# Kernel optimization log

Measured on AMD Instinct MI355X. Metric: run time of the kernel, lower is better.

The kernel has to match this reference:

```python
import jax, jax.numpy as jnp
import numpy as np

B, S, Db, E, T = 64, 512, 768, 50, 68
NC, NT, K, V = 16, 8, 3, 100
MAXLEN = 8


def _make_spans(k1, k2, n):
    starts = jax.random.randint(k1, (B, n), 0, S - MAXLEN)
    lens = jax.random.randint(k2, (B, n), 1, MAXLEN + 1)
    return jnp.stack([starts, starts + lens], axis=-1)  # [B,n,2] half-open


def setup_inputs() -> dict:
    key = jax.random.key(0)
    ks = jax.random.split(key, 12)
    enc = jax.random.normal(ks[0], (B, S, Db), jnp.float32)
    entity_table = jax.random.normal(ks[1], (V, E), jnp.float32) * 0.02
    entity_table = entity_table.at[0].set(0.0)  # padding_idx=0
    fc1_w = jax.random.normal(ks[2], (Db, Db + E), jnp.float32) * 0.02
    fc1_b = jnp.zeros((Db,), jnp.float32)
    trig_w = jax.random.normal(ks[3], (T, Db), jnp.float32) * 0.02
    trig_b = jnp.zeros((T,), jnp.float32)
    entities_x = jax.random.randint(ks[4], (B, S, K), 0, V)
    head_idx = jax.random.randint(ks[5], (B, S), 0, S)
    cand_spans = _make_spans(ks[6], ks[7], NC)
    trig_spans = _make_spans(ks[8], ks[9], NT)
    return {"enc": enc, "entity_table": entity_table, "fc1_w": fc1_w,
            "fc1_b": fc1_b, "trig_w": trig_w, "trig_b": trig_b,
            "entities_x": entities_x, "head_idx": head_idx,
            "cand_spans": cand_spans, "trig_spans": trig_spans}


def _span_mean(x, spans):
    # x: [B,S,D], spans: [B,N,2] half-open -> [B,N,D] mean over span tokens
    pos = jnp.arange(x.shape[1])
    mask = (pos[None, None, :] >= spans[..., 0:1]) & (pos[None, None, :] < spans[..., 1:2])
    m = mask.astype(x.dtype)  # [B,N,S]
    cnt = jnp.maximum(m.sum(-1, keepdims=True), 1.0)
    return jnp.einsum('bns,bsd->bnd', m, x) / cnt


def reference(enc, entity_table, fc1_w, fc1_b, trig_w, trig_b,
              entities_x, head_idx, cand_spans, trig_spans):
    # multi-label entity embedding: sum over K label slots (padding row is zero)
    ent = entity_table[entities_x].sum(axis=2)            # [B,S,E]
    x = jnp.concatenate([enc, ent], axis=-1)              # [B,S,Db+E]
    x = jax.nn.relu(jnp.einsum('bsd,hd->bsh', x, fc1_w) + fc1_b)  # fc1 (dropout=eval)
    # per-sample index_select over sequence dim (wordpiece head gather)
    x = jnp.take_along_axis(x, head_idx[:, :, None], axis=1)      # [B,S,768]
    trigger_logits = jnp.einsum('bsh,th->bst', x, trig_w) + trig_b  # [B,S,T]
    trigger_hat = jnp.argmax(trigger_logits, axis=-1)
    # span mean-pooling for predicted triggers and golden entity candidates
    ev = _span_mean(x, trig_spans)                        # [B,NT,768]
    en = _span_mean(x, cand_spans)                        # [B,NC,768]
    ev_e = jnp.broadcast_to(ev[:, :, None, :], (B, NT, NC, Db))
    en_e = jnp.broadcast_to(en[:, None, :, :], (B, NT, NC, Db))
    argument_hidden = jnp.concatenate([ev_e, en_e], axis=-1)  # [B,NT,NC,1536]
    return trigger_logits, trigger_hat, argument_hidden
```

## Files before the change

kernel.cpp:

```cpp
#include <hip/hip_runtime.h>

#define BS_TOTAL 32768
#define DB 768
#define KV 832
#define KREAL 818
#define TT 68
#define SEQ 512

typedef float v2f __attribute__((ext_vector_type(2)));
typedef float f32x4 __attribute__((ext_vector_type(4)));
typedef _Float16 f16x8 __attribute__((ext_vector_type(8)));
typedef _Float16 f16x4 __attribute__((ext_vector_type(4)));
typedef unsigned int uint;
typedef unsigned short ushort;

union U4 { uint4 u; f16x8 h; };

__device__ __forceinline__ _Float16 us2h(ushort x){ union{ushort u;_Float16 h;}c; c.u=x; return c.h; }
__device__ __forceinline__ ushort h2us(_Float16 x){ union{ushort u;_Float16 h;}c; c.h=x; return c.u; }
__device__ __forceinline__ uint packx(float xs){
    _Float16 h=(_Float16)xs; _Float16 l=(_Float16)(xs-(float)h);
    return (uint)h2us(h) | ((uint)h2us(l)<<16);
}

__global__ __launch_bounds__(256) void splitw_kernel(
    const float* __restrict__ W, const float* __restrict__ Wt,
    _Float16* __restrict__ W0, _Float16* __restrict__ W1,
    _Float16* __restrict__ T0, _Float16* __restrict__ T1)
{
    int row = blockIdx.x;
    int t = threadIdx.x;
    if (row < DB) {
        int c4 = t * 4;
        if (c4 < KV) {
#pragma unroll
            for (int j = 0; j < 4; ++j) {
                int k = c4 + j;
                float v = (k < KREAL) ? W[(size_t)row * KREAL + k] * 1024.f : 0.f;
                _Float16 h = (_Float16)v;
                W0[(size_t)row * KV + k] = h;
                W1[(size_t)row * KV + k] = (_Float16)(v - (float)h);
            }
        }
    } else {
        int r2 = row - DB;
#pragma unroll
        for (int j = 0; j < 3; ++j) {
            int k = t * 3 + j;
            if (k < DB) {
                float v = (r2 < TT) ? Wt[(size_t)r2 * DB + k] * 1024.f : 0.f;
                _Float16 h = (_Float16)v;
                T0[(size_t)r2 * DB + k] = h;
                T1[(size_t)r2 * DB + k] = (_Float16)(v - (float)h);
            }
        }
    }
}

__global__ __launch_bounds__(256, 2) void fc1_mfma(
    const float* __restrict__ enc, const int* __restrict__ ex,
    const float* __restrict__ table,
    const _Float16* __restrict__ W0, const _Float16* __restrict__ W1,
    const float* __restrict__ bias, uint* __restrict__ xout)
{
    __shared__ char lds[65536];
    char* sA0 = lds;
    char* sA1 = lds + 16384;
    char* sW0 = lds + 32768;
    char* sW1 = lds + 49152;
    const int t = threadIdx.x;
    const int l = t & 63;
    const int w = t >> 6;
    const int wr = w >> 1, wc = w & 1;
    const int bm0 = blockIdx.x * 128;
    const int bn0 = blockIdx.y * 128;

    f32x4 acc[4][4];
#pragma unroll
    for (int i = 0; i < 4; ++i)
#pragma unroll
        for (int j = 0; j < 4; ++j) acc[i][j] = (f32x4){0.f, 0.f, 0.f, 0.f};

    float4 pa[8];
    uint4 pw0[4], pw1[4];

    auto loadA = [&](int k0) {
        if (k0 < DB) {
#pragma unroll
            for (int c = 0; c < 8; ++c) {
                int idx = t + c * 256;
                int r = idx >> 4;
                int c4 = (idx & 15) << 2;
                pa[c] = *reinterpret_cast<const float4*>(enc + (size_t)(bm0 + r) * DB + k0 + c4);
            }
        } else {
#pragma unroll
            for (int c = 0; c < 8; ++c) {
                int idx = t + c * 256;
                int r = idx >> 4;
                int c4 = (idx & 15) << 2;
                const int* exr = ex + (size_t)(bm0 + r) * 3;
                int i0 = exr[0] * 50, i1 = exr[1] * 50, i2 = exr[2] * 50;
                float vv[4];
#pragma unroll
                for (int j = 0; j < 4; ++j) {
                    int e = c4 + j;
                    vv[j] = (e < 50) ? (table[i0 + e] + table[i1 + e] + table[i2 + e]) : 0.f;
                }
                pa[c] = make_float4(vv[0], vv[1], vv[2], vv[3]);
            }
        }
    };
    auto loadW = [&](int k0) {
#pragma unroll
        for (int c = 0; c < 4; ++c) {
            int idx = t + c * 256;
            int r = idx >> 3;
            int h0 = (idx & 7) << 3;
            pw0[c] = *reinterpret_cast<const uint4*>(W0 + (size_t)(bn0 + r) * KV + k0 + h0);
            pw1[c] = *reinterpret_cast<const uint4*>(W1 + (size_t)(bn0 + r) * KV + k0 + h0);
        }
    };

    loadA(0); loadW(0);

    for (int kt = 0; kt < 13; ++kt) {
        __syncthreads();
#pragma unroll
        for (int c = 0; c < 8; ++c) {
            int idx = t + c * 256;
            int r = idx >> 4;
            int b0 = (idx & 15) << 3;
            int off = (r << 7) + (b0 ^ ((r & 7) << 4));
            float f0 = pa[c].x * 32.f, f1 = pa[c].y * 32.f;
            float f2 = pa[c].z * 32.f, f3 = pa[c].w * 32.f;
            _Float16 h0 = (_Float16)f0, h1 = (_Float16)f1, h2 = (_Float16)f2, h3 = (_Float16)f3;
            f16x4 hi = {h0, h1, h2, h3};
            f16x4 lo = {(_Float16)(f0 - (float)h0), (_Float16)(f1 - (float)h1),
                        (_Float16)(f2 - (float)h2), (_Float16)(f3 - (float)h3)};
            *reinterpret_cast<f16x4*>(sA0 + off) = hi;
            *reinterpret_cast<f16x4*>(sA1 + off) = lo;
        }
#pragma unroll
        for (int c = 0; c < 4; ++c) {
            int idx = t + c * 256;
            int r = idx >> 3;
            int b0 = (idx & 7) << 4;
            int off = (r << 7) + (b0 ^ ((r & 7) << 4));
            *reinterpret_cast<uint4*>(sW0 + off) = pw0[c];
            *reinterpret_cast<uint4*>(sW1 + off) = pw1[c];
        }
        __syncthreads();
        if (kt < 12) { loadA((kt + 1) * 64); loadW((kt + 1) * 64); }
#pragma unroll
        for (int ks = 0; ks < 2; ++ks) {
            const int lr = l & 15;
            const int kb = ks * 64 + ((l >> 4) << 4);
            f16x8 a0f[4], a1f[4], b0f[4], b1f[4];
#pragma unroll
            for (int mf = 0; mf < 4; ++mf) {
                int r = wr * 64 + mf * 16 + lr;
                int off = (r << 7) + (kb ^ ((r & 7) << 4));
                a0f[mf] = *reinterpret_cast<const f16x8*>(sA0 + off);
                a1f[mf] = *reinterpret_cast<const f16x8*>(sA1 + off);
            }
#pragma unroll
            for (int nf = 0; nf < 4; ++nf) {
                int r = wc * 64 + nf * 16 + lr;
                int off = (r << 7) + (kb ^ ((r & 7) << 4));
                b0f[nf] = *reinterpret_cast<const f16x8*>(sW0 + off);
                b1f[nf] = *reinterpret_cast<const f16x8*>(sW1 + off);
            }
#pragma unroll
            for (int mf = 0; mf < 4; ++mf)
#pragma unroll
                for (int nf = 0; nf < 4; ++nf) {
                    acc[mf][nf] = __builtin_amdgcn_mfma_f32_16x16x32_f16(a0f[mf], b0f[nf], acc[mf][nf], 0, 0, 0);
                    acc[mf][nf] = __builtin_amdgcn_mfma_f32_16x16x32_f16(a1f[mf], b0f[nf], acc[mf][nf], 0, 0, 0);
                    acc[mf][nf] = __builtin_amdgcn_mfma_f32_16x16x32_f16(a0f[mf], b1f[nf], acc[mf][nf], 0, 0, 0);
                }
        }
    }

    const float inv = 1.0f / 32768.f;
#pragma unroll
    for (int nf = 0; nf < 4; ++nf) {
        int col = bn0 + wc * 64 + nf * 16 + (l & 15);
        float bv = bias[col];
#pragma unroll
        for (int mf = 0; mf < 4; ++mf) {
            int rbase = bm0 + wr * 64 + mf * 16 + ((l >> 4) << 2);
#pragma unroll
            for (int j = 0; j < 4; ++j) {
                float x = fmaxf(acc[mf][nf][j] * inv + bv, 0.f);
                xout[(size_t)(rbase + j) * DB + col] = packx(x * 256.f);
            }
        }
    }
}

__global__ __launch_bounds__(256, 4) void trig_mfma(
    const uint* __restrict__ xfc, const int* __restrict__ head_idx,
    const _Float16* __restrict__ T0, const _Float16* __restrict__ T1,
    const float* __restrict__ bt, float* __restrict__ logits, float* __restrict__ hat)
{
    __shared__ char sA[16384];
    __shared__ char sW[20480];
    __shared__ int srow[64];
    const int t = threadIdx.x;
    const int l = t & 63;
    const int w = t >> 6;
    const int lr = l & 15, hi2 = l >> 4;
    const int s0 = blockIdx.x * 64;
    if (t < 64) srow[t] = (((s0 + t) >> 9) << 9) + head_idx[s0 + t];
    __syncthreads();

    f32x4 acc[5];
#pragma unroll
    for (int n = 0; n < 5; ++n) acc[n] = (f32x4){0.f, 0.f, 0.f, 0.f};

    uint4 pa[4];
    uint4 pw[5];

    auto loadA = [&](int k0) {
        int r = t >> 2, c16 = (t & 3) << 4;
        const uint* src = xfc + (size_t)srow[r] * DB + k0 + c16;
#pragma unroll
        for (int q = 0; q < 4; ++q) pa[q] = *reinterpret_cast<const uint4*>(src + q * 4);
    };
    auto loadW = [&](int k0) {
#pragma unroll
        for (int i = 0; i < 5; ++i) {
            int cid = t + i * 256;
            int row = cid >> 4;
            int sl = cid & 15;
            const _Float16* src = ((sl >> 3) ? T1 : T0) + (size_t)row * DB + k0 + (sl & 7) * 8;
            pw[i] = *reinterpret_cast<const uint4*>(src);
        }
    };

    loadA(0); loadW(0);

    for (int kt = 0; kt < 12; ++kt) {
        __syncthreads();
        {
            int r = t >> 2, c16 = (t & 3) << 4;
            int sw = (r & 7) << 4;
            uint uu[16];
#pragma unroll
            for (int q = 0; q < 4; ++q) *reinterpret_cast<uint4*>(uu + q * 4) = pa[q];
            U4 h0, h1, l0, l1;
#pragma unroll
            for (int j = 0; j < 8; ++j) {
                h0.h[j] = us2h((ushort)(uu[j] & 0xffff));
                l0.h[j] = us2h((ushort)(uu[j] >> 16));
                h1.h[j] = us2h((ushort)(uu[8 + j] & 0xffff));
                l1.h[j] = us2h((ushort)(uu[8 + j] >> 16));
            }
            int bh = c16 * 2;
            *reinterpret_cast<uint4*>(sA + (r << 8) + ((bh +  0) ^ sw)) = h0.u;
            *reinterpret_cast<uint4*>(sA + (r << 8) + ((bh + 16) ^ sw)) = h1.u;
            *reinterpret_cast<uint4*>(sA + (r << 8) + (128 + ((bh +  0) ^ sw))) = l0.u;
            *reinterpret_cast<uint4*>(sA + (r << 8) + (128 + ((bh + 16) ^ sw))) = l1.u;
        }
#pragma unroll
        for (int i = 0; i < 5; ++i) {
            int cid = t + i * 256;
            int row = cid >> 4;
            int sl = cid & 15;
            int sw = (row & 7) << 4;
            int byte = (sl >> 3) * 128 + (((sl & 7) * 16) ^ sw);
            *reinterpret_cast<uint4*>(sW + (row << 8) + byte) = pw[i];
        }
        __syncthreads();
        if (kt < 11) { loadA((kt + 1) * 64); loadW((kt + 1) * 64); }
#pragma unroll
        for (int ks = 0; ks < 2; ++ks) {
            int hb = ks * 64 + hi2 * 16;
            int rA = w * 16 + lr;
            int swA = (rA & 7) << 4;
            f16x8 ah = *reinterpret_cast<const f16x8*>(sA + (rA << 8) + (hb ^ swA));
            f16x8 al = *reinterpret_cast<const f16x8*>(sA + (rA << 8) + (128 + (hb ^ swA)));
#pragma unroll
            for (int nf = 0; nf < 5; ++nf) {
                int rB = nf * 16 + lr;
                int swB = (rB & 7) << 4;
                f16x8 bh = *reinterpret_cast<const f16x8*>(sW + (rB << 8) + (hb ^ swB));
                f16x8 bl = *reinterpret_cast<const f16x8*>(sW + (rB << 8) + (128 + (hb ^ swB)));
                acc[nf] = __builtin_amdgcn_mfma_f32_16x16x32_f16(ah, bh, acc[nf], 0, 0, 0);
                acc[nf] = __builtin_amdgcn_mfma_f32_16x16x32_f16(al, bh, acc[nf], 0, 0, 0);
                acc[nf] = __builtin_amdgcn_mfma_f32_16x16x32_f16(ah, bl, acc[nf], 0, 0, 0);
            }
        }
    }

    const float inv = 1.0f / 262144.f;
#pragma unroll
    for (int j = 0; j < 4; ++j) {
        int row = s0 + w * 16 + hi2 * 4 + j;
        float bestv = -1e38f;
        int besti = 0;
#pragma unroll
        for (int nf = 0; nf < 5; ++nf) {
            int col = nf * 16 + lr;
            float v = -1e38f;
            if (col < TT) {
                v = acc[nf][j] * inv + bt[col];
                logits[(size_t)row * TT + col] = v;
            }
            if (v > bestv) { bestv = v; besti = col; }
        }
#pragma unroll
        for (int off = 8; off > 0; off >>= 1) {
            float ov = __shfl_xor(bestv, off, 16);
            int oi = __shfl_xor(besti, off, 16);
            if (ov > bestv || (ov == bestv && oi < besti)) { bestv = ov; besti = oi; }
        }
        if (lr == 0) hat[row] = (float)besti;
    }
}

__global__ __launch_bounds__(256) void pool_kernel(
    const uint* __restrict__ xfc, const int* __restrict__ head_idx,
    const int* __restrict__ cand_spans, const int* __restrict__ trig_spans,
    float* __restrict__ pooled)
{
    const int n = blockIdx.x;
    const int b = blockIdx.y;
    __shared__ int sh_rows[8];
    __shared__ int sh_len;
    __shared__ int sh_st;
    __shared__ float sh_inv;
    const int t = threadIdx.x;
    if (t == 0) {
        const int* sp = (n < 8) ? (trig_spans + (b * 8 + n) * 2)
                                : (cand_spans + (b * 16 + (n - 8)) * 2);
        int st = sp[0], en = sp[1];
        int len = en - st;
        if (len < 0) len = 0;
        if (len > 8) len = 8;
        sh_len = len;
        sh_st = st;
        sh_inv = (1.f / (float)(len > 0 ? len : 1)) * (1.f / 256.f);
    }
    __syncthreads();
    if (t < sh_len) sh_rows[t] = (b << 9) + head_idx[(b << 9) + sh_st + t];
    __syncthreads();
    const int len = sh_len;
    const float inv = sh_inv;
#pragma unroll
    for (int j = 0; j < 3; ++j) {
        int c = t + j * 256;
        float s = 0.f;
        for (int p = 0; p < len; ++p) {
            uint u = xfc[(size_t)sh_rows[p] * DB + c];
            s += (float)us2h((ushort)(u & 0xffff)) + (float)us2h((ushort)(u >> 16));
        }
        pooled[((size_t)b * 24 + n) * DB + c] = s * inv;
    }
}

__global__ __launch_bounds__(256) void arg_kernel(
    const float* __restrict__ pooled, float* __restrict__ out2)
{
    int g = blockIdx.x * 256 + threadIdx.x;
    int b = g / 49152;
    int rem = g - b * 49152;
    int pair = rem / 384;
    int off4 = rem - pair * 384;
    int ti = pair >> 4;
    int c = pair & 15;
    int col = off4 << 2;
    const float* src;
    if (col < DB) src = pooled + ((size_t)(b * 24 + ti)) * DB + col;
    else          src = pooled + ((size_t)(b * 24 + 8 + c)) * DB + (col - DB);
    float4 v = *reinterpret_cast<const float4*>(src);
    *reinterpret_cast<float4*>(out2 + ((size_t)g << 2)) = v;
}

extern "C" void kernel_launch(void* const* d_in, const int* in_sizes, int n_in,
                              void* d_out, int out_size, void* d_ws, size_t ws_size,
                              hipStream_t stream)
{
    const float* enc   = (const float*)d_in[0];
    const float* table = (const float*)d_in[1];
    const float* fc1w  = (const float*)d_in[2];
    const float* fc1b  = (const float*)d_in[3];
    const float* trigw = (const float*)d_in[4];
    const float* trigb = (const float*)d_in[5];
    const int*   ex    = (const int*)d_in[6];
    const int*   hidx  = (const int*)d_in[7];
    const int*   cspan = (const int*)d_in[8];
    const int*   tspan = (const int*)d_in[9];

    float* out0 = (float*)d_out;
    float* out1 = out0 + (size_t)BS_TOTAL * TT;
    float* out2 = out1 + BS_TOTAL;

    uint*  ws_xfc  = (uint*)d_ws;
    float* ws_pool = (float*)(ws_xfc + (size_t)BS_TOTAL * DB);
    _Float16* wsW0 = (_Float16*)(ws_pool + (size_t)64 * 24 * DB);
    _Float16* wsW1 = wsW0 + (size_t)DB * KV;
    _Float16* wsT0 = wsW1 + (size_t)DB * KV;
    _Float16* wsT1 = wsT0 + (size_t)80 * DB;

    splitw_kernel<<<dim3(DB + 80), dim3(256), 0, stream>>>(fc1w, trigw, wsW0, wsW1, wsT0, wsT1);
    fc1_mfma<<<dim3(BS_TOTAL / 128, DB / 128), dim3(256), 0, stream>>>(
        enc, ex, table, wsW0, wsW1, fc1b, ws_xfc);
    trig_mfma<<<dim3(BS_TOTAL / 64), dim3(256), 0, stream>>>(
        ws_xfc, hidx, wsT0, wsT1, trigb, out0, out1);
    pool_kernel<<<dim3(24, 64), dim3(256), 0, stream>>>(ws_xfc, hidx, cspan, tspan, ws_pool);
    arg_kernel<<<dim3(3145728 / 256), dim3(256), 0, stream>>>(ws_pool, out2);
}
```

Baseline: 279.2 us.

## Prepack fc1 weights in MFMA fragment order and stage output stores through LDS

```diff
diff --git a/kernel.cpp b/kernel.cpp
--- a/kernel.cpp
+++ b/kernel.cpp
@@ -23,57 +23,65 @@
     return (uint)h2us(h) | ((uint)h2us(l)<<16);
 }
 
-__global__ __launch_bounds__(256) void splitw_kernel(
-    const float* __restrict__ W, const float* __restrict__ Wt,
-    _Float16* __restrict__ W0, _Float16* __restrict__ W1,
-    _Float16* __restrict__ T0, _Float16* __restrict__ T1)
-{
-    int row = blockIdx.x;
+__global__ __launch_bounds__(64) void packwf_kernel(
+    const float* __restrict__ W, _Float16* __restrict__ Wf)
+{
+    const int bid = blockIdx.x;
+    const int l = threadIdx.x;
+    const int bn = bid / 208;
+    const int rem = bid % 208;
+    const int kt = rem >> 4;
+    const int sub = rem & 15;
+    const int ks = sub >> 3;
+    const int nfg = sub & 7;
+    const int row = bn * 128 + nfg * 16 + (l & 15);
+    const int kb = kt * 64 + ks * 32 + ((l >> 4) << 3);
+    f16x8 hi, lo;
+#pragma unroll
+    for (int q = 0; q < 8; ++q) {
+        int k = kb + q;
+        float v = (k < KREAL) ? W[(size_t)row * KREAL + k] * 1024.f : 0.f;
+        _Float16 h = (_Float16)v;
+        hi[q] = h; lo[q] = (_Float16)(v - (float)h);
+    }
+    const size_t fb = ((((size_t)bn * 13 + kt) * 2 + ks) * 8 + nfg) * 2;
+    *reinterpret_cast<f16x8*>(Wf + (fb + 0) * 512 + l * 8) = hi;
+    *reinterpret_cast<f16x8*>(Wf + (fb + 1) * 512 + l * 8) = lo;
+}
+
+__global__ __launch_bounds__(256) void splitw_trig(
+    const float* __restrict__ Wt, _Float16* __restrict__ T0, _Float16* __restrict__ T1)
+{
+    int r2 = blockIdx.x;
     int t = threadIdx.x;
-    if (row < DB) {
-        int c4 = t * 4;
-        if (c4 < KV) {
-#pragma unroll
-            for (int j = 0; j < 4; ++j) {
-                int k = c4 + j;
-                float v = (k < KREAL) ? W[(size_t)row * KREAL + k] * 1024.f : 0.f;
-                _Float16 h = (_Float16)v;
-                W0[(size_t)row * KV + k] = h;
-                W1[(size_t)row * KV + k] = (_Float16)(v - (float)h);
-            }
-        }
-    } else {
-        int r2 = row - DB;
-#pragma unroll
-        for (int j = 0; j < 3; ++j) {
-            int k = t * 3 + j;
-            if (k < DB) {
-                float v = (r2 < TT) ? Wt[(size_t)r2 * DB + k] * 1024.f : 0.f;
-                _Float16 h = (_Float16)v;
-                T0[(size_t)r2 * DB + k] = h;
-                T1[(size_t)r2 * DB + k] = (_Float16)(v - (float)h);
-            }
+#pragma unroll
+    for (int j = 0; j < 3; ++j) {
+        int k = t * 3 + j;
+        if (k < DB) {
+            float v = (r2 < TT) ? Wt[(size_t)r2 * DB + k] * 1024.f : 0.f;
+            _Float16 h = (_Float16)v;
+            T0[(size_t)r2 * DB + k] = h;
+            T1[(size_t)r2 * DB + k] = (_Float16)(v - (float)h);
         }
     }
 }
 
 __global__ __launch_bounds__(256, 2) void fc1_mfma(
     const float* __restrict__ enc, const int* __restrict__ ex,
-    const float* __restrict__ table,
-    const _Float16* __restrict__ W0, const _Float16* __restrict__ W1,
+    const float* __restrict__ table, const _Float16* __restrict__ Wf,
     const float* __restrict__ bias, uint* __restrict__ xout)
 {
-    __shared__ char lds[65536];
+    __shared__ char lds[32768];
     char* sA0 = lds;
     char* sA1 = lds + 16384;
-    char* sW0 = lds + 32768;
-    char* sW1 = lds + 49152;
     const int t = threadIdx.x;
     const int l = t & 63;
     const int w = t >> 6;
     const int wr = w >> 1, wc = w & 1;
+    const int lr = l & 15, hi2 = l >> 4;
     const int bm0 = blockIdx.x * 128;
-    const int bn0 = blockIdx.y * 128;
+    const int by = blockIdx.y;
+    const int bn0 = by * 128;
 
     f32x4 acc[4][4];
 #pragma unroll
@@ -82,7 +90,7 @@
         for (int j = 0; j < 4; ++j) acc[i][j] = (f32x4){0.f, 0.f, 0.f, 0.f};
 
     float4 pa[8];
-    uint4 pw0[4], pw1[4];
+    uint4 bf[8];
 
     auto loadA = [&](int k0) {
         if (k0 < DB) {
@@ -111,18 +119,15 @@
             }
         }
     };
-    auto loadW = [&](int k0) {
-#pragma unroll
-        for (int c = 0; c < 4; ++c) {
-            int idx = t + c * 256;
-            int r = idx >> 3;
-            int h0 = (idx & 7) << 3;
-            pw0[c] = *reinterpret_cast<const uint4*>(W0 + (size_t)(bn0 + r) * KV + k0 + h0);
-            pw1[c] = *reinterpret_cast<const uint4*>(W1 + (size_t)(bn0 + r) * KV + k0 + h0);
-        }
+    auto loadBf = [&](int kt, int ks) {
+        const size_t fb = ((((size_t)by * 13 + kt) * 2 + ks) * 8 + wc * 4) * 2;
+        const _Float16* base = Wf + fb * 512 + l * 8;
+#pragma unroll
+        for (int q = 0; q < 8; ++q)
+            bf[q] = *reinterpret_cast<const uint4*>(base + (size_t)q * 512);
     };
 
-    loadA(0); loadW(0);
+    loadA(0); loadBf(0, 0);
 
     for (int kt = 0; kt < 13; ++kt) {
         __syncthreads();
@@ -141,21 +146,11 @@
             *reinterpret_cast<f16x4*>(sA0 + off) = hi;
             *reinterpret_cast<f16x4*>(sA1 + off) = lo;
         }
-#pragma unroll
-        for (int c = 0; c < 4; ++c) {
-            int idx = t + c * 256;
-            int r = idx >> 3;
-            int b0 = (idx & 7) << 4;
-            int off = (r << 7) + (b0 ^ ((r & 7) << 4));
-            *reinterpret_cast<uint4*>(sW0 + off) = pw0[c];
-            *reinterpret_cast<uint4*>(sW1 + off) = pw1[c];
-        }
-        __syncthreads();
-        if (kt < 12) { loadA((kt + 1) * 64); loadW((kt + 1) * 64); }
+        __syncthreads();
+        if (kt < 12) loadA((kt + 1) * 64);
 #pragma unroll
         for (int ks = 0; ks < 2; ++ks) {
-            const int lr = l & 15;
-            const int kb = ks * 64 + ((l >> 4) << 4);
+            const int kb = ks * 64 + (hi2 << 4);
             f16x8 a0f[4], a1f[4], b0f[4], b1f[4];
 #pragma unroll
             for (int mf = 0; mf < 4; ++mf) {
@@ -166,11 +161,14 @@
             }
 #pragma unroll
             for (int nf = 0; nf < 4; ++nf) {
-                int r = wc * 64 + nf * 16 + lr;
-                int off = (r << 7) + (kb ^ ((r & 7) << 4));
-                b0f[nf] = *reinterpret_cast<const f16x8*>(sW0 + off);
-                b1f[nf] = *reinterpret_cast<const f16x8*>(sW1 + off);
-            }
+                U4 u0, u1;
+                u0.u = bf[nf * 2 + 0];
+                u1.u = bf[nf * 2 + 1];
+                b0f[nf] = u0.h;
+                b1f[nf] = u1.h;
+            }
+            if (ks == 0) loadBf(kt, 1);
+            else if (kt < 12) loadBf(kt + 1, 0);
 #pragma unroll
             for (int mf = 0; mf < 4; ++mf)
 #pragma unroll
@@ -182,20 +180,39 @@
         }
     }
 
-    const float inv = 1.0f / 32768.f;
-#pragma unroll
-    for (int nf = 0; nf < 4; ++nf) {
-        int col = bn0 + wc * 64 + nf * 16 + (l & 15);
-        float bv = bias[col];
-#pragma unroll
-        for (int mf = 0; mf < 4; ++mf) {
-            int rbase = bm0 + wr * 64 + mf * 16 + ((l >> 4) << 2);
-#pragma unroll
-            for (int j = 0; j < 4; ++j) {
-                float x = fmaxf(acc[mf][nf][j] * inv + bv, 0.f);
-                xout[(size_t)(rbase + j) * DB + col] = packx(x * 256.f);
-            }
-        }
+    const float inv0 = 1.0f / 32768.f;
+    uint* sE = reinterpret_cast<uint*>(lds);
+    float bv[4];
+#pragma unroll
+    for (int nf = 0; nf < 4; ++nf) bv[nf] = bias[bn0 + wc * 64 + nf * 16 + lr];
+
+#pragma unroll
+    for (int p = 0; p < 4; ++p) {
+        __syncthreads();
+        if (wr == (p >> 1)) {
+#pragma unroll
+            for (int mi = 0; mi < 2; ++mi) {
+                int mf = (p & 1) * 2 + mi;
+                int rowl = mf * 16 + hi2 * 4 - (p & 1) * 32;
+#pragma unroll
+                for (int nf = 0; nf < 4; ++nf) {
+                    int col = wc * 64 + nf * 16 + lr;
+#pragma unroll
+                    for (int j = 0; j < 4; ++j) {
+                        float x = fmaxf(acc[mf][nf][j] * inv0 + bv[nf], 0.f);
+                        sE[(rowl + j) * 132 + col] = packx(x * 256.f);
+                    }
+                }
+            }
+        }
+        __syncthreads();
+        int rrow = t >> 3;
+        int c0 = (t & 7) << 4;
+        uint* gp = xout + (size_t)(bm0 + p * 32 + rrow) * DB + bn0 + c0;
+        const uint* sp = sE + rrow * 132 + c0;
+#pragma unroll
+        for (int q = 0; q < 4; ++q)
+            *reinterpret_cast<uint4*>(gp + q * 4) = *reinterpret_cast<const uint4*>(sp + q * 4);
     }
 }
 
@@ -399,14 +416,14 @@
 
     uint*  ws_xfc  = (uint*)d_ws;
     float* ws_pool = (float*)(ws_xfc + (size_t)BS_TOTAL * DB);
-    _Float16* wsW0 = (_Float16*)(ws_pool + (size_t)64 * 24 * DB);
-    _Float16* wsW1 = wsW0 + (size_t)DB * KV;
-    _Float16* wsT0 = wsW1 + (size_t)DB * KV;
+    _Float16* wsWf = (_Float16*)(ws_pool + (size_t)64 * 24 * DB);
+    _Float16* wsT0 = wsWf + (size_t)2496 * 512;
     _Float16* wsT1 = wsT0 + (size_t)80 * DB;
 
-    splitw_kernel<<<dim3(DB + 80), dim3(256), 0, stream>>>(fc1w, trigw, wsW0, wsW1, wsT0, wsT1);
+    packwf_kernel<<<dim3(1248), dim3(64), 0, stream>>>(fc1w, wsWf);
+    splitw_trig<<<dim3(80), dim3(256), 0, stream>>>(trigw, wsT0, wsT1);
     fc1_mfma<<<dim3(BS_TOTAL / 128, DB / 128), dim3(256), 0, stream>>>(
-        enc, ex, table, wsW0, wsW1, fc1b, ws_xfc);
+        enc, ex, table, wsWf, fc1b, ws_xfc);
     trig_mfma<<<dim3(BS_TOTAL / 64), dim3(256), 0, stream>>>(
         ws_xfc, hidx, wsT0, wsT1, trigb, out0, out1);
     pool_kernel<<<dim3(24, 64), dim3(256), 0, stream>>>(ws_xfc, hidx, cspan, tspan, ws_pool);
```

Result: faster. 250.4 us (-10.3%).
